# Performance work log

Hardware: AMD Instinct MI355X
Metric: run time of the kernel (lower is better)

The kernel has to match this reference:

```python
import jax, jax.numpy as jnp
import numpy as np

B, T, E, H = 4, 2048, 1024, 16
D = E // H  # head dim = 64


def setup_inputs() -> dict:
    key = jax.random.key(0)
    k1, k2, k3 = jax.random.split(key, 3)
    g = jax.random.normal(k1, (B, T, E), dtype=jnp.float32)
    W_lift = jax.random.normal(k2, (2 * E, E), dtype=jnp.float32) * (1.0 / np.sqrt(E))
    W_proj = jax.random.normal(k3, (H, H), dtype=jnp.float32) * (1.0 / np.sqrt(H))
    return {"g": g, "W_lift": W_lift, "W_proj": W_proj}


def reference(g, W_lift, W_proj):
    b, t, e = g.shape
    h, d = H, e // H
    # lift: Linear(E, 2E, bias=False) -> split into q, k
    qk = jnp.einsum('bte,fe->btf', g, W_lift)  # (B, T, 2E)
    q, k = qk[..., :e], qk[..., e:]
    q = q.reshape(b, t, h, d).transpose(0, 2, 1, 3)  # (B, H, T, D)
    k = k.reshape(b, t, h, d).transpose(0, 2, 1, 3)  # (B, H, T, D)
    # unscaled causal scores
    a = jnp.einsum('bhqd,bhkd->bhqk', q, k)  # (B, H, T, T)
    causal = jnp.tril(jnp.ones((t, t), dtype=bool))
    a = jnp.where(causal[None, None], a, -jnp.inf)
    # masked logsumexp over key dim -> (B, H, T)
    lse = jax.scipy.special.logsumexp(a, axis=-1)
    out = lse.transpose(0, 2, 1)  # (B, T, H)
    out = jnp.einsum('bth,gh->btg', out, W_proj)  # proj Linear(H, H)
    out = out.sum(axis=2)  # (B, T)
    return out.reshape(-1, out.shape[-1])
```

## Files before the change

kernel.cpp:

```cpp
#include <hip/hip_runtime.h>
#include <hip/hip_bf16.h>

#define B_ 4
#define T_ 2048
#define E_ 1024
#define H_ 16
#define D_ 64
#define Mtot 8192
#define N2 2048
#define K_ 1024
#define PS_ (B_ * H_ * T_)

typedef __attribute__((ext_vector_type(8))) short short8;
typedef __attribute__((ext_vector_type(4))) float f32x4;
using bf16 = __hip_bfloat16;

__device__ __forceinline__ void async_copy16(const void* g, void* l) {
  __builtin_amdgcn_global_load_lds(
      (const __attribute__((address_space(1))) unsigned int*)g,
      (__attribute__((address_space(3))) unsigned int*)l, 16, 0, 0);
}

__global__ void cast_f32_to_bf16(const float* __restrict__ in, ushort* __restrict__ out, int n4) {
  int stride = gridDim.x * blockDim.x;
  for (int i = blockIdx.x * blockDim.x + threadIdx.x; i < n4; i += stride) {
    float4 v = reinterpret_cast<const float4*>(in)[i];
    bf16 a = __float2bfloat16(v.x), b = __float2bfloat16(v.y);
    bf16 c = __float2bfloat16(v.z), d = __float2bfloat16(v.w);
    ushort4 o = make_ushort4(*(ushort*)&a, *(ushort*)&b, *(ushort*)&c, *(ushort*)&d);
    reinterpret_cast<ushort4*>(out)[i] = o;
  }
}

#define GBK 64

__launch_bounds__(256)
__global__ void lift_gemm(const bf16* __restrict__ A, const bf16* __restrict__ Bm,
                          bf16* __restrict__ qh, bf16* __restrict__ kh) {
  __shared__ __align__(16) bf16 sA[128 * GBK];
  __shared__ __align__(16) bf16 sB[128 * GBK];
  const int m0 = blockIdx.x * 128;
  const int n0 = blockIdx.y * 128;
  const int tid = threadIdx.x;
  const int lane = tid & 63, w = tid >> 6;
  const int wr = w >> 1, wc = w & 1;
  const int lr = lane & 15, lg = lane >> 4;

  f32x4 acc[4][4];
#pragma unroll
  for (int i = 0; i < 4; ++i)
#pragma unroll
    for (int j = 0; j < 4; ++j) acc[i][j] = (f32x4)(0.0f);

  const char* Ab = (const char*)A;
  const char* Bb = (const char*)Bm;

  for (int k0 = 0; k0 < K_; k0 += GBK) {
    __syncthreads();
#pragma unroll
    for (int it = 0; it < 4; ++it) {
      const int o = ((w * 4 + it) << 10) | (lane << 4);
      const int lin = o ^ (((o >> 7) & 7) << 4);
      const int r = lin >> 7, cb = lin & 127;
      const size_t gof = ((size_t)(m0 + r) * K_ + k0) * 2 + cb;
      const size_t gof_b = ((size_t)(n0 + r) * K_ + k0) * 2 + cb;
      async_copy16(Ab + gof, (char*)sA + ((w * 4 + it) << 10));
      async_copy16(Bb + gof_b, (char*)sB + ((w * 4 + it) << 10));
    }
    __syncthreads();

#pragma unroll
    for (int h = 0; h < 2; ++h) {
      short8 af[4], bfr[4];
#pragma unroll
      for (int i = 0; i < 4; ++i) {
        int row = wr * 64 + i * 16 + lr;
        int off = (row << 7) + (h << 6) + (lg << 4);
        off ^= ((row & 7) << 4);
        af[i] = *(const short8*)((const char*)sA + off);
      }
#pragma unroll
      for (int j = 0; j < 4; ++j) {
        int row = wc * 64 + j * 16 + lr;
        int off = (row << 7) + (h << 6) + (lg << 4);
        off ^= ((row & 7) << 4);
        bfr[j] = *(const short8*)((const char*)sB + off);
      }
#pragma unroll
      for (int i = 0; i < 4; ++i)
#pragma unroll
        for (int j = 0; j < 4; ++j)
          acc[i][j] = __builtin_amdgcn_mfma_f32_16x16x32_bf16(af[i], bfr[j], acc[i][j], 0, 0, 0);
    }
  }

#pragma unroll
  for (int i = 0; i < 4; ++i) {
#pragma unroll
    for (int j = 0; j < 4; ++j) {
#pragma unroll
      for (int r = 0; r < 4; ++r) {
        int m = m0 + wr * 64 + i * 16 + lg * 4 + r;
        int f = n0 + wc * 64 + j * 16 + lr;
        bf16 bv = __float2bfloat16(acc[i][j][r]);
        int b = m >> 11, t = m & (T_ - 1);
        int hh = (f & (E_ - 1)) >> 6, d = f & (D_ - 1);
        bf16* dst = (f < E_) ? qh : kh;
        dst[((((size_t)b * H_ + hh) * T_) + t) * D_ + d] = bv;
      }
    }
  }
}

#define LSE_QT 128

__launch_bounds__(256)
__global__ void attn_lse(const bf16* __restrict__ qh, const bf16* __restrict__ kh,
                         float* __restrict__ psum) {
  __shared__ __align__(16) bf16 sK[2][64 * 64];
  const int bid = blockIdx.x;
  const int qt = 15 - (bid >> 8);
  const int rem = bid & 255;
  const int bh = rem >> 2;
  const int s = rem & 3;
  const int tid = threadIdx.x;
  const int lane = tid & 63, w = tid >> 6;
  const int lr = lane & 15, lg = lane >> 4;
  const int qbase = qt * LSE_QT + w * 32;

  const bf16* qp = qh + ((size_t)bh * T_ + qbase) * D_;
  short8 qf[2][2];
#pragma unroll
  for (int f = 0; f < 2; ++f)
#pragma unroll
    for (int h = 0; h < 2; ++h)
      qf[f][h] = *(const short8*)&qp[(size_t)(f * 16 + lr) * D_ + h * 32 + lg * 8];

  float l[2][4];
#pragma unroll
  for (int f = 0; f < 2; ++f)
#pragma unroll
    for (int r = 0; r < 4; ++r) l[f][r] = 0.0f;

  const char* kbase = (const char*)(kh + (size_t)bh * T_ * D_);
  const int nfullw = qt * 2 + (w >> 1);
  const int maxk = qt * 2 + 1;
  const int nt = (s <= maxk) ? ((maxk - s) >> 2) + 1 : 0;

#define STAGE_K(bi, kt_)                                                      \
  do {                                                                        \
    const char* kp_ = kbase + (size_t)(kt_) * (64 * D_ * 2);                  \
    _Pragma("unroll") for (int it = 0; it < 2; ++it) {                        \
      const int o = ((w * 2 + it) << 10) | (lane << 4);                       \
      const int lin = o ^ (((o >> 7) & 7) << 4);                              \
      async_copy16(kp_ + lin, (char*)&sK[bi][0] + ((w * 2 + it) << 10));      \
    }                                                                         \
  } while (0)

  int cur = 0;
  if (nt > 0) STAGE_K(0, s);
  for (int i = 0; i < nt; ++i) {
    __syncthreads();
    if (i + 1 < nt) STAGE_K(cur ^ 1, s + 4 * (i + 1));
    const int kt = s + 4 * i;
    if (kt <= nfullw) {
      const char* kb = (const char*)&sK[cur][0];
      short8 kf[4][2];
#pragma unroll
      for (int j = 0; j < 4; ++j) {
        int row = j * 16 + lr;
        int sw = ((row & 7) << 4);
        kf[j][0] = *(const short8*)(kb + (((row << 7) | (lg << 4)) ^ sw));
        kf[j][1] = *(const short8*)(kb + (((row << 7) | 64 | (lg << 4)) ^ sw));
      }
      f32x4 sc[2][4];
#pragma unroll
      for (int f = 0; f < 2; ++f)
#pragma unroll
        for (int j = 0; j < 4; ++j) sc[f][j] = (f32x4)(0.0f);
#pragma unroll
      for (int j = 0; j < 4; ++j) {
        sc[0][j] = __builtin_amdgcn_mfma_f32_16x16x32_bf16(qf[0][0], kf[j][0], sc[0][j], 0, 0, 0);
        sc[0][j] = __builtin_amdgcn_mfma_f32_16x16x32_bf16(qf[0][1], kf[j][1], sc[0][j], 0, 0, 0);
        sc[1][j] = __builtin_amdgcn_mfma_f32_16x16x32_bf16(qf[1][0], kf[j][0], sc[1][j], 0, 0, 0);
        sc[1][j] = __builtin_amdgcn_mfma_f32_16x16x32_bf16(qf[1][1], kf[j][1], sc[1][j], 0, 0, 0);
      }
      if (kt < nfullw) {
#pragma unroll
        for (int f = 0; f < 2; ++f)
#pragma unroll
          for (int j = 0; j < 4; ++j)
#pragma unroll
            for (int r = 0; r < 4; ++r) l[f][r] += __expf(sc[f][j][r]);
      } else {
#pragma unroll
        for (int f = 0; f < 2; ++f)
#pragma unroll
          for (int j = 0; j < 4; ++j)
#pragma unroll
            for (int r = 0; r < 4; ++r) {
              int qrow = qbase + f * 16 + lg * 4 + r;
              int key = kt * 64 + j * 16 + lr;
              float a = (key <= qrow) ? sc[f][j][r] : -INFINITY;
              l[f][r] += __expf(a);
            }
      }
    }
    __syncthreads();
    cur ^= 1;
  }

#pragma unroll
  for (int f = 0; f < 2; ++f)
#pragma unroll
    for (int r = 0; r < 4; ++r) {
      float v = l[f][r];
      v += __shfl_xor(v, 1);
      v += __shfl_xor(v, 2);
      v += __shfl_xor(v, 4);
      v += __shfl_xor(v, 8);
      if (lr == 0)
        psum[(size_t)s * PS_ + (size_t)bh * T_ + qbase + f * 16 + lg * 4 + r] = v;
    }
}

__global__ void proj_out(const float* __restrict__ psum, const float* __restrict__ Wp,
                         float* __restrict__ out) {
  __shared__ float cw[H_];
  int tid = threadIdx.x;
  if (tid < H_) {
    float s = 0.0f;
    for (int g = 0; g < H_; ++g) s += Wp[g * H_ + tid];
    cw[tid] = s;
  }
  __syncthreads();
  int idx = blockIdx.x * blockDim.x + tid;
  int b = idx >> 11, t = idx & (T_ - 1);
  float acc = 0.0f;
#pragma unroll
  for (int h = 0; h < H_; ++h) {
    size_t base = ((size_t)(b * H_ + h) * T_) + t;
    float v = psum[base] + psum[PS_ + base] + psum[2 * (size_t)PS_ + base] +
              psum[3 * (size_t)PS_ + base];
    acc += __logf(v) * cw[h];
  }
  out[idx] = acc;
}

extern "C" void kernel_launch(void* const* d_in, const int* in_sizes, int n_in,
                              void* d_out, int out_size, void* d_ws, size_t ws_size,
                              hipStream_t stream) {
  (void)in_sizes; (void)n_in; (void)out_size; (void)ws_size;
  const float* g  = (const float*)d_in[0];
  const float* Wl = (const float*)d_in[1];
  const float* Wp = (const float*)d_in[2];
  float* out = (float*)d_out;

  char* ws = (char*)d_ws;
  size_t off = 0;
  bf16* g_bf  = (bf16*)(ws + off); off += (size_t)Mtot * K_ * 2;
  bf16* wl_bf = (bf16*)(ws + off); off += (size_t)N2 * K_ * 2;
  bf16* qh    = (bf16*)(ws + off); off += (size_t)B_ * H_ * T_ * D_ * 2;
  bf16* kh    = (bf16*)(ws + off); off += (size_t)B_ * H_ * T_ * D_ * 2;
  float* psum = (float*)(ws + off);

  cast_f32_to_bf16<<<2048, 256, 0, stream>>>(g,  (ushort*)g_bf,  (Mtot * K_) / 4);
  cast_f32_to_bf16<<<512,  256, 0, stream>>>(Wl, (ushort*)wl_bf, (N2 * K_) / 4);

  lift_gemm<<<dim3(Mtot / 128, N2 / 128), 256, 0, stream>>>(g_bf, wl_bf, qh, kh);

  attn_lse<<<4096, 256, 0, stream>>>(qh, kh, psum);

  proj_out<<<(B_ * T_) / 256, 256, 0, stream>>>(psum, Wp, out);
}
```

Baseline: 99.17 us.

## Rewrite lift GEMM as 256x256 double-buffered pipelined tile with 8 waves

The lift GEMM moves from 128x128 tiles with 4 waves and a load-then-compute loop to 256x256 tiles with 8 waves. It double-buffers LDS and prefetches the next k-tile's A and B halves while MFMAs run on the current tile. It also adds block-index swizzling for L2 locality, setprio around MFMA bursts, and sched barriers to control the interleaving. The aim is to hide global-load latency and cut per-block overhead, at the cost of 128KB LDS, more accumulator registers, and fewer blocks (256 blocks).

```diff
diff --git a/kernel.cpp b/kernel.cpp
--- a/kernel.cpp
+++ b/kernel.cpp
@@ -10,6 +10,7 @@
 #define N2 2048
 #define K_ 1024
 #define PS_ (B_ * H_ * T_)
+#define NKT 16
 
 typedef __attribute__((ext_vector_type(8))) short short8;
 typedef __attribute__((ext_vector_type(4))) float f32x4;
@@ -32,77 +33,153 @@
   }
 }
 
-#define GBK 64
-
-__launch_bounds__(256)
+#define MFMA_BF16(a, b, c) __builtin_amdgcn_mfma_f32_16x16x32_bf16(a, b, c, 0, 0, 0)
+
+__launch_bounds__(512, 2)
 __global__ void lift_gemm(const bf16* __restrict__ A, const bf16* __restrict__ Bm,
                           bf16* __restrict__ qh, bf16* __restrict__ kh) {
-  __shared__ __align__(16) bf16 sA[128 * GBK];
-  __shared__ __align__(16) bf16 sB[128 * GBK];
-  const int m0 = blockIdx.x * 128;
-  const int n0 = blockIdx.y * 128;
+  __shared__ __align__(16) char sL[8][16384];
+  const int bid = blockIdx.x;
+  const int swz = ((bid & 7) << 5) | (bid >> 3);
+  const int m0 = (swz >> 3) * 256;
+  const int n0 = (swz & 7) * 256;
   const int tid = threadIdx.x;
   const int lane = tid & 63, w = tid >> 6;
-  const int wr = w >> 1, wc = w & 1;
+  const int wm = w >> 2, wn = w & 3;
   const int lr = lane & 15, lg = lane >> 4;
 
-  f32x4 acc[4][4];
-#pragma unroll
-  for (int i = 0; i < 4; ++i)
+  f32x4 acc[8][4];
+#pragma unroll
+  for (int i = 0; i < 8; ++i)
 #pragma unroll
     for (int j = 0; j < 4; ++j) acc[i][j] = (f32x4)(0.0f);
 
-  const char* Ab = (const char*)A;
-  const char* Bb = (const char*)Bm;
-
-  for (int k0 = 0; k0 < K_; k0 += GBK) {
-    __syncthreads();
-#pragma unroll
-    for (int it = 0; it < 4; ++it) {
-      const int o = ((w * 4 + it) << 10) | (lane << 4);
+  auto stage_half = [&](int slot, const bf16* gsrc, int Rbase, int kcol) {
+#pragma unroll
+    for (int it = 0; it < 2; ++it) {
+      const int o = ((it * 512 + tid) << 4);
       const int lin = o ^ (((o >> 7) & 7) << 4);
       const int r = lin >> 7, cb = lin & 127;
-      const size_t gof = ((size_t)(m0 + r) * K_ + k0) * 2 + cb;
-      const size_t gof_b = ((size_t)(n0 + r) * K_ + k0) * 2 + cb;
-      async_copy16(Ab + gof, (char*)sA + ((w * 4 + it) << 10));
-      async_copy16(Bb + gof_b, (char*)sB + ((w * 4 + it) << 10));
-    }
-    __syncthreads();
-
-#pragma unroll
-    for (int h = 0; h < 2; ++h) {
-      short8 af[4], bfr[4];
-#pragma unroll
-      for (int i = 0; i < 4; ++i) {
-        int row = wr * 64 + i * 16 + lr;
-        int off = (row << 7) + (h << 6) + (lg << 4);
-        off ^= ((row & 7) << 4);
-        af[i] = *(const short8*)((const char*)sA + off);
-      }
-#pragma unroll
-      for (int j = 0; j < 4; ++j) {
-        int row = wc * 64 + j * 16 + lr;
-        int off = (row << 7) + (h << 6) + (lg << 4);
-        off ^= ((row & 7) << 4);
-        bfr[j] = *(const short8*)((const char*)sB + off);
-      }
-#pragma unroll
-      for (int i = 0; i < 4; ++i)
-#pragma unroll
-        for (int j = 0; j < 4; ++j)
-          acc[i][j] = __builtin_amdgcn_mfma_f32_16x16x32_bf16(af[i], bfr[j], acc[i][j], 0, 0, 0);
-    }
-  }
-
-#pragma unroll
-  for (int i = 0; i < 4; ++i) {
-#pragma unroll
-    for (int j = 0; j < 4; ++j) {
+      async_copy16((const char*)gsrc + ((size_t)(Rbase + r) * K_ + kcol) * 2 + cb,
+                   &sL[slot][o]);
+    }
+  };
+  auto rd = [&](int slot, int row, int khalf) -> short8 {
+    int off = (row << 7) + (khalf << 6) + (lg << 4);
+    off ^= (row & 7) << 4;
+    return *(const short8*)&sL[slot][off];
+  };
+
+  stage_half(0, A, m0, 0);
+  stage_half(1, A, m0 + 128, 0);
+  stage_half(2, Bm, n0, 0);
+  stage_half(3, Bm, n0 + 128, 0);
+
+  short8 af[4][2], bf0[2][2], bf1[2][2];
+
+  for (int kt = 0; kt < NKT; ++kt) {
+    const int cb = (kt & 1) << 2;
+    const int nb = cb ^ 4;
+    const int kcol = (kt + 1) * 64;
+    const int aslot = cb + wm;
+    const int bslot = cb + 2 + (wn >> 1);
+    const int brow = (wn & 1) * 64;
+
+    if (kt + 1 < NKT) {
+      stage_half(nb + 0, A, m0, kcol);
+      stage_half(nb + 1, A, m0 + 128, kcol);
+      asm volatile("s_waitcnt vmcnt(4)" ::: "memory");
+    } else {
+      asm volatile("s_waitcnt vmcnt(0)" ::: "memory");
+    }
+    __builtin_amdgcn_sched_barrier(0);
+    __builtin_amdgcn_s_barrier();
+#pragma unroll
+    for (int i = 0; i < 4; ++i) {
+      af[i][0] = rd(aslot, i * 16 + lr, 0);
+      af[i][1] = rd(aslot, i * 16 + lr, 1);
+    }
+#pragma unroll
+    for (int j = 0; j < 2; ++j) {
+      bf0[j][0] = rd(bslot, brow + j * 16 + lr, 0);
+      bf0[j][1] = rd(bslot, brow + j * 16 + lr, 1);
+    }
+    __builtin_amdgcn_s_setprio(1);
+#pragma unroll
+    for (int i = 0; i < 4; ++i)
+#pragma unroll
+      for (int j = 0; j < 2; ++j) {
+        acc[i][j] = MFMA_BF16(af[i][0], bf0[j][0], acc[i][j]);
+        acc[i][j] = MFMA_BF16(af[i][1], bf0[j][1], acc[i][j]);
+      }
+    __builtin_amdgcn_s_setprio(0);
+    __builtin_amdgcn_sched_barrier(0);
+    __builtin_amdgcn_s_barrier();
+
+    if (kt + 1 < NKT) {
+      stage_half(nb + 2, Bm, n0, kcol);
+      stage_half(nb + 3, Bm, n0 + 128, kcol);
+    }
+#pragma unroll
+    for (int j = 0; j < 2; ++j) {
+      bf1[j][0] = rd(bslot, brow + (j + 2) * 16 + lr, 0);
+      bf1[j][1] = rd(bslot, brow + (j + 2) * 16 + lr, 1);
+    }
+    __builtin_amdgcn_sched_barrier(0);
+    __builtin_amdgcn_s_barrier();
+    __builtin_amdgcn_s_setprio(1);
+#pragma unroll
+    for (int i = 0; i < 4; ++i)
+#pragma unroll
+      for (int j = 0; j < 2; ++j) {
+        acc[i][j + 2] = MFMA_BF16(af[i][0], bf1[j][0], acc[i][j + 2]);
+        acc[i][j + 2] = MFMA_BF16(af[i][1], bf1[j][1], acc[i][j + 2]);
+      }
+    __builtin_amdgcn_s_setprio(0);
+    __builtin_amdgcn_sched_barrier(0);
+    __builtin_amdgcn_s_barrier();
+
+#pragma unroll
+    for (int i = 0; i < 4; ++i) {
+      af[i][0] = rd(aslot, (i + 4) * 16 + lr, 0);
+      af[i][1] = rd(aslot, (i + 4) * 16 + lr, 1);
+    }
+    __builtin_amdgcn_sched_barrier(0);
+    __builtin_amdgcn_s_barrier();
+    __builtin_amdgcn_s_setprio(1);
+#pragma unroll
+    for (int i = 0; i < 4; ++i)
+#pragma unroll
+      for (int j = 0; j < 2; ++j) {
+        acc[i + 4][j] = MFMA_BF16(af[i][0], bf0[j][0], acc[i + 4][j]);
+        acc[i + 4][j] = MFMA_BF16(af[i][1], bf0[j][1], acc[i + 4][j]);
+      }
+    __builtin_amdgcn_s_setprio(0);
+    __builtin_amdgcn_sched_barrier(0);
+    __builtin_amdgcn_s_barrier();
+
+    __builtin_amdgcn_s_setprio(1);
+#pragma unroll
+    for (int i = 0; i < 4; ++i)
+#pragma unroll
+      for (int j = 0; j < 2; ++j) {
+        acc[i + 4][j + 2] = MFMA_BF16(af[i][0], bf1[j][0], acc[i + 4][j + 2]);
+        acc[i + 4][j + 2] = MFMA_BF16(af[i][1], bf1[j][1], acc[i + 4][j + 2]);
+      }
+    __builtin_amdgcn_s_setprio(0);
+    __builtin_amdgcn_sched_barrier(0);
+    __builtin_amdgcn_s_barrier();
+  }
+
+#pragma unroll
+  for (int mi = 0; mi < 8; ++mi) {
+#pragma unroll
+    for (int ni = 0; ni < 4; ++ni) {
 #pragma unroll
       for (int r = 0; r < 4; ++r) {
-        int m = m0 + wr * 64 + i * 16 + lg * 4 + r;
-        int f = n0 + wc * 64 + j * 16 + lr;
-        bf16 bv = __float2bfloat16(acc[i][j][r]);
+        int m = m0 + wm * 128 + mi * 16 + lg * 4 + r;
+        int f = n0 + wn * 64 + ni * 16 + lr;
+        bf16 bv = __float2bfloat16(acc[mi][ni][r]);
         int b = m >> 11, t = m & (T_ - 1);
         int hh = (f & (E_ - 1)) >> 6, d = f & (D_ - 1);
         bf16* dst = (f < E_) ? qh : kh;
@@ -180,10 +257,10 @@
         for (int j = 0; j < 4; ++j) sc[f][j] = (f32x4)(0.0f);
 #pragma unroll
       for (int j = 0; j < 4; ++j) {
-        sc[0][j] = __builtin_amdgcn_mfma_f32_16x16x32_bf16(qf[0][0], kf[j][0], sc[0][j], 0, 0, 0);
-        sc[0][j] = __builtin_amdgcn_mfma_f32_16x16x32_bf16(qf[0][1], kf[j][1], sc[0][j], 0, 0, 0);
-        sc[1][j] = __builtin_amdgcn_mfma_f32_16x16x32_bf16(qf[1][0], kf[j][0], sc[1][j], 0, 0, 0);
-        sc[1][j] = __builtin_amdgcn_mfma_f32_16x16x32_bf16(qf[1][1], kf[j][1], sc[1][j], 0, 0, 0);
+        sc[0][j] = MFMA_BF16(qf[0][0], kf[j][0], sc[0][j]);
+        sc[0][j] = MFMA_BF16(qf[0][1], kf[j][1], sc[0][j]);
+        sc[1][j] = MFMA_BF16(qf[1][0], kf[j][0], sc[1][j]);
+        sc[1][j] = MFMA_BF16(qf[1][1], kf[j][1], sc[1][j]);
       }
       if (kt < nfullw) {
 #pragma unroll
@@ -267,7 +344,7 @@
   cast_f32_to_bf16<<<2048, 256, 0, stream>>>(g,  (ushort*)g_bf,  (Mtot * K_) / 4);
   cast_f32_to_bf16<<<512,  256, 0, stream>>>(Wl, (ushort*)wl_bf, (N2 * K_) / 4);
 
-  lift_gemm<<<dim3(Mtot / 128, N2 / 128), 256, 0, stream>>>(g_bf, wl_bf, qh, kh);
+  lift_gemm<<<256, 512, 0, stream>>>(g_bf, wl_bf, qh, kh);
 
   attn_lse<<<4096, 256, 0, stream>>>(qh, kh, psum);
 
```

Result: faster. 92.01 us (-7.2%).
